# Kernel tuning notes

Measured on AMD Instinct MI355X. Metric: run time of the kernel, lower is better.

Reference implementation:

```python
import jax, jax.numpy as jnp
import numpy as np

BN_EPS = 1e-5
NN_EPS = 1e-8
K = 3


def conv_bn_relu(x, W, b, gamma, beta, mean, var):
    # x: [B, Cin, N]; W: [Cout, Cin] (1x1 conv); BN in inference mode w/ running stats
    y = jnp.einsum('bcn,oc->bon', x, W) + b[None, :, None]
    y = (y - mean[None, :, None]) * (gamma / jnp.sqrt(var + BN_EPS))[None, :, None] + beta[None, :, None]
    return jax.nn.relu(y)


def three_interpolation(p1, p2, f2):
    # p1: [B, N1, 3] unknown xyz; p2: [B, N2, 3] known xyz; f2: [B, C, N2]
    # squared pairwise distances via the expansion trick (avoids [B,N1,N2,3])
    d2 = (jnp.sum(p1 * p1, -1)[:, :, None]
          + jnp.sum(p2 * p2, -1)[:, None, :]
          - 2.0 * jnp.einsum('bnd,bmd->bnm', p1, p2))  # [B, N1, N2]
    neg_d2, idx = jax.lax.top_k(-d2, K)                 # 3 nearest
    dist = -neg_d2                                      # squared dists, [B, N1, 3]
    recip = 1.0 / (dist + NN_EPS)
    weight = recip / jnp.sum(recip, axis=-1, keepdims=True)  # [B, N1, 3]
    f2t = jnp.transpose(f2, (0, 2, 1))                  # [B, N2, C]
    gathered = jax.vmap(lambda f, i: f[i])(f2t, idx)    # [B, N1, 3, C]
    return jnp.einsum('bnkc,bnk->bcn', gathered, weight)  # [B, C, N1]


def setup_inputs() -> dict:
    key = jax.random.key(0)
    ks = jax.random.split(key, 16)
    B, N1, N2 = 8, 16384, 4096
    mlp = [256, 128, 128]
    inp = {
        'p1': jax.random.normal(ks[0], (B, N1, 3), jnp.float32),
        'p2': jax.random.normal(ks[1], (B, N2, 3), jnp.float32),
        'f2': jax.random.normal(ks[2], (B, mlp[0], N2), jnp.float32),
    }
    kidx = 3
    for li in range(len(mlp) - 1):
        cin, cout = mlp[li], mlp[li + 1]
        inp[f'W{li}'] = jax.random.normal(ks[kidx], (cout, cin), jnp.float32) * (1.0 / np.sqrt(cin)); kidx += 1
        inp[f'b{li}'] = jnp.zeros((cout,), jnp.float32)
        inp[f'gamma{li}'] = jnp.ones((cout,), jnp.float32)
        inp[f'beta{li}'] = jnp.zeros((cout,), jnp.float32)
        inp[f'mean{li}'] = jax.random.normal(ks[kidx], (cout,), jnp.float32) * 0.1; kidx += 1
        inp[f'var{li}'] = jax.random.uniform(ks[kidx], (cout,), jnp.float32, 0.5, 1.5); kidx += 1
    return inp


def reference(p1, p2, f2,
              W0, b0, gamma0, beta0, mean0, var0,
              W1, b1, gamma1, beta1, mean1, var1):
    f = conv_bn_relu(f2, W0, b0, gamma0, beta0, mean0, var0)
    f = conv_bn_relu(f, W1, b1, gamma1, beta1, mean1, var1)
    return three_interpolation(p1, p2, f)
```

## Files before the change

### kernel.cpp

```cpp
#include <hip/hip_runtime.h>

#define B_    8
#define N1_   16384
#define N2_   4096
#define NTOT_ (B_ * N1_)

__device__ __forceinline__ float np_sumsq(float x, float y, float z)
{
#pragma clang fp contract(off)
    return ((x * x + y * y) + z * z);
}

__global__ __launch_bounds__(256) void fold_kernel(
    const float* __restrict__ W, const float* __restrict__ bias,
    const float* __restrict__ gamma, const float* __restrict__ beta,
    const float* __restrict__ mean, const float* __restrict__ var,
    float* __restrict__ Wp, float* __restrict__ bp, int Cout, int Cin)
{
    int t = blockIdx.x * 256 + threadIdx.x;
    if (t < Cout * Cin) {
        int o = t / Cin;
        float s = gamma[o] / sqrtf(var[o] + 1e-5f);
        Wp[t] = W[t] * s;
    }
    if (t < Cout) {
        float s = gamma[t] / sqrtf(var[t] + 1e-5f);
        bp[t] = beta[t] + (bias[t] - mean[t]) * s;
    }
}

__global__ __launch_bounds__(256) void q4_kernel(
    const float* __restrict__ p2, float4* __restrict__ q4)
{
    int t = blockIdx.x * 256 + threadIdx.x;
    float x = p2[3 * (size_t)t + 0];
    float y = p2[3 * (size_t)t + 1];
    float z = p2[3 * (size_t)t + 2];
    q4[t] = make_float4(x, y, z, np_sumsq(x, y, z));
}

template <int CIN, bool TRANS>
__global__ __launch_bounds__(256) void gemm_relu_kernel(
    const float* __restrict__ X, const float* __restrict__ Wp,
    const float* __restrict__ bp, float* __restrict__ Y)
{
    __shared__ float A_lds[32][136];
    __shared__ float B_lds[32][128];

    const int b  = blockIdx.y;
    const int n0 = blockIdx.x * 128;
    const int tid = threadIdx.x;
    const int ty = tid >> 4;
    const int tx = tid & 15;
    const float* Xb = X + (size_t)b * CIN * N2_;

    float acc[8][8];
#pragma unroll
    for (int i = 0; i < 8; ++i)
#pragma unroll
        for (int j = 0; j < 8; ++j) acc[i][j] = 0.f;

    const int a_kq = (tid & 7) * 4;
    const int a_r0 = tid >> 3;
    const int b_n4 = (tid & 31) * 4;
    const int b_k0 = tid >> 5;

    for (int k0 = 0; k0 < CIN; k0 += 32) {
#pragma unroll
        for (int i = 0; i < 4; ++i) {
            const int row = a_r0 + 32 * i;
            const float4 v = *(const float4*)&Wp[(size_t)row * CIN + k0 + a_kq];
            A_lds[a_kq + 0][row] = v.x;
            A_lds[a_kq + 1][row] = v.y;
            A_lds[a_kq + 2][row] = v.z;
            A_lds[a_kq + 3][row] = v.w;
        }
#pragma unroll
        for (int i = 0; i < 4; ++i) {
            const int krow = b_k0 + 8 * i;
            *(float4*)&B_lds[krow][b_n4] =
                *(const float4*)&Xb[(size_t)(k0 + krow) * N2_ + n0 + b_n4];
        }
        __syncthreads();

#pragma unroll
        for (int kk = 0; kk < 32; ++kk) {
            const float4 a0 = *(const float4*)&A_lds[kk][ty * 4];
            const float4 a1 = *(const float4*)&A_lds[kk][64 + ty * 4];
            const float4 bq0 = *(const float4*)&B_lds[kk][tx * 4];
            const float4 bq1 = *(const float4*)&B_lds[kk][64 + tx * 4];
            const float av[8] = {a0.x, a0.y, a0.z, a0.w, a1.x, a1.y, a1.z, a1.w};
            const float bv[8] = {bq0.x, bq0.y, bq0.z, bq0.w, bq1.x, bq1.y, bq1.z, bq1.w};
#pragma unroll
            for (int i = 0; i < 8; ++i)
#pragma unroll
                for (int j = 0; j < 8; ++j)
                    acc[i][j] = fmaf(av[i], bv[j], acc[i][j]);
        }
        __syncthreads();
    }

    float bias_v[8];
#pragma unroll
    for (int i = 0; i < 8; ++i) {
        const int r = (i < 4) ? (ty * 4 + i) : (64 + ty * 4 + (i - 4));
        bias_v[i] = bp[r];
    }

    if (!TRANS) {
#pragma unroll
        for (int i = 0; i < 8; ++i) {
            const int r = (i < 4) ? (ty * 4 + i) : (64 + ty * 4 + (i - 4));
            float* yrow = Y + ((size_t)b * 128 + r) * N2_ + n0;
            float4 v0, v1;
            v0.x = fmaxf(acc[i][0] + bias_v[i], 0.f);
            v0.y = fmaxf(acc[i][1] + bias_v[i], 0.f);
            v0.z = fmaxf(acc[i][2] + bias_v[i], 0.f);
            v0.w = fmaxf(acc[i][3] + bias_v[i], 0.f);
            v1.x = fmaxf(acc[i][4] + bias_v[i], 0.f);
            v1.y = fmaxf(acc[i][5] + bias_v[i], 0.f);
            v1.z = fmaxf(acc[i][6] + bias_v[i], 0.f);
            v1.w = fmaxf(acc[i][7] + bias_v[i], 0.f);
            *(float4*)(yrow + tx * 4) = v0;
            *(float4*)(yrow + 64 + tx * 4) = v1;
        }
    } else {
        float (*T)[132] = (float(*)[132])&A_lds[0][0];
#pragma unroll
        for (int s = 0; s < 4; ++s) {
            if ((tx >> 3) == (s & 1)) {
                const int joff = (s >> 1) * 4;
                const int cl0 = (tx & 7) * 4;
#pragma unroll
                for (int i = 0; i < 8; ++i) {
                    const int r = (i < 4) ? (ty * 4 + i) : (64 + ty * 4 + (i - 4));
#pragma unroll
                    for (int j = 0; j < 4; ++j)
                        T[cl0 + j][r] = fmaxf(acc[i][j + joff] + bias_v[i], 0.f);
                }
            }
            __syncthreads();
#pragma unroll
            for (int p = 0; p < 4; ++p) {
                const int row = (tid >> 5) + 8 * p;
                const float4 v = *(const float4*)&T[row][(tid & 31) * 4];
                float* orow = Y + ((size_t)b * N2_ + n0 + 32 * s + row) * 128;
                *(float4*)&orow[(tid & 31) * 4] = v;
            }
            __syncthreads();
        }
    }
}

__global__ __launch_bounds__(256, 8) void knn_phase1(
    const float* __restrict__ p1, const float4* __restrict__ q4,
    float* __restrict__ part_d, int* __restrict__ part_i)
{
    __shared__ float4 qs[1024];
    const int tid = threadIdx.x;
    const int chunk = blockIdx.x & 3;
    const int g = (blockIdx.x >> 2) * 256 + tid;
    const int b = g >> 14;

    const float px = p1[3 * (size_t)g + 0];
    const float py = p1[3 * (size_t)g + 1];
    const float pz = p1[3 * (size_t)g + 2];
    const float s1 = np_sumsq(px, py, pz);

    const float4* qb = q4 + (size_t)b * N2_ + chunk * 1024;
#pragma unroll
    for (int i = 0; i < 4; ++i) qs[tid + i * 256] = qb[tid + i * 256];
    __syncthreads();

    float d0 = 1e30f, d1 = 1e30f, d2v = 1e30f;
    int i0 = 0, i1 = 0, i2 = 0;
    const int jbase = chunk * 1024;

    for (int j = 0; j < 1024; j += 4) {
#pragma unroll
        for (int u = 0; u < 4; ++u) {
            const float4 q = qs[j + u];
            const float dot = __fmaf_rn(px, q.x, __fmaf_rn(py, q.y, __fmul_rn(pz, q.z)));
            const float ss  = s1 + q.w;
            const float t   = __fmaf_rn(-2.0f, dot, ss);
            if (t < d2v) {
                const int jj = jbase + j + u;
                const bool c1 = t < d1, c0 = t < d0;
                d2v = c1 ? d1 : t;                 i2 = c1 ? i1 : jj;
                const float nd1 = c1 ? (c0 ? d0 : t) : d1;
                const int   ni1 = c1 ? (c0 ? i0 : jj) : i1;
                d1 = nd1;                          i1 = ni1;
                d0 = c0 ? t : d0;                  i0 = c0 ? jj : i0;
            }
        }
    }

    part_d[(0 * 4 + chunk) * NTOT_ + g] = d0;
    part_d[(1 * 4 + chunk) * NTOT_ + g] = d1;
    part_d[(2 * 4 + chunk) * NTOT_ + g] = d2v;
    part_i[(0 * 4 + chunk) * NTOT_ + g] = i0;
    part_i[(1 * 4 + chunk) * NTOT_ + g] = i1;
    part_i[(2 * 4 + chunk) * NTOT_ + g] = i2;
}

__global__ __launch_bounds__(256) void knn_merge(
    const float* __restrict__ part_d, const int* __restrict__ part_i,
    int* __restrict__ idx_ws, float* __restrict__ w_ws)
{
    const int g = blockIdx.x * 256 + threadIdx.x;

    float d0 = 1e30f, d1 = 1e30f, d2v = 1e30f;
    int i0 = 0, i1 = 0, i2 = 0;

#pragma unroll
    for (int c = 0; c < 4; ++c) {
#pragma unroll
        for (int k = 0; k < 3; ++k) {
            const float t = part_d[(k * 4 + c) * NTOT_ + g];
            const int  jj = part_i[(k * 4 + c) * NTOT_ + g];
            if (t < d2v) {
                const bool c1 = t < d1, c0 = t < d0;
                d2v = c1 ? d1 : t;                 i2 = c1 ? i1 : jj;
                const float nd1 = c1 ? (c0 ? d0 : t) : d1;
                const int   ni1 = c1 ? (c0 ? i0 : jj) : i1;
                d1 = nd1;                          i1 = ni1;
                d0 = c0 ? t : d0;                  i0 = c0 ? jj : i0;
            }
        }
    }

    float w0, w1, w2;
    {
#pragma clang fp contract(off)
        const float r0 = 1.0f / (d0 + 1e-8f);
        const float r1 = 1.0f / (d1 + 1e-8f);
        const float r2 = 1.0f / (d2v + 1e-8f);
        const float rs = (r0 + r1) + r2;
        w0 = r0 / rs;
        w1 = r1 / rs;
        w2 = r2 / rs;
    }

    idx_ws[g]             = i0;
    idx_ws[NTOT_ + g]     = i1;
    idx_ws[2 * NTOT_ + g] = i2;
    w_ws[g]               = w0;
    w_ws[NTOT_ + g]       = w1;
    w_ws[2 * NTOT_ + g]   = w2;
}

__global__ __launch_bounds__(256) void gather_kernel(
    const float* __restrict__ f_t, const int* __restrict__ idx_ws,
    const float* __restrict__ w_ws, float* __restrict__ out)
{
    const int tid = threadIdx.x;
    const int lane = tid & 63, cg = tid >> 6;
    const int g = blockIdx.x * 64 + lane;
    const int b = g >> 14, n = g & 16383;

    const int i0 = idx_ws[g];
    const int i1 = idx_ws[NTOT_ + g];
    const int i2 = idx_ws[2 * NTOT_ + g];
    const float w0 = w_ws[g];
    const float w1 = w_ws[NTOT_ + g];
    const float w2 = w_ws[2 * NTOT_ + g];

    const float* base = f_t + (size_t)b * N2_ * 128 + cg * 32;
    const float4* r0 = (const float4*)(base + (size_t)i0 * 128);
    const float4* r1 = (const float4*)(base + (size_t)i1 * 128);
    const float4* r2 = (const float4*)(base + (size_t)i2 * 128);

    float acc[32];
#pragma unroll
    for (int q = 0; q < 8; ++q) {
        const float4 a = r0[q], bb = r1[q], c = r2[q];
        acc[4 * q + 0] = fmaf(w0, a.x, fmaf(w1, bb.x, w2 * c.x));
        acc[4 * q + 1] = fmaf(w0, a.y, fmaf(w1, bb.y, w2 * c.y));
        acc[4 * q + 2] = fmaf(w0, a.z, fmaf(w1, bb.z, w2 * c.z));
        acc[4 * q + 3] = fmaf(w0, a.w, fmaf(w1, bb.w, w2 * c.w));
    }

    float* ob = out + ((size_t)b * 128 + cg * 32) * N1_ + n;
#pragma unroll
    for (int c = 0; c < 32; ++c)
        __builtin_nontemporal_store(acc[c], ob + (size_t)c * N1_);
}

extern "C" void kernel_launch(void* const* d_in, const int* in_sizes, int n_in,
                              void* d_out, int out_size, void* d_ws, size_t ws_size,
                              hipStream_t stream)
{
    const float* p1  = (const float*)d_in[0];
    const float* p2  = (const float*)d_in[1];
    const float* f2  = (const float*)d_in[2];
    const float* W0  = (const float*)d_in[3];
    const float* b0  = (const float*)d_in[4];
    const float* g0  = (const float*)d_in[5];
    const float* be0 = (const float*)d_in[6];
    const float* m0  = (const float*)d_in[7];
    const float* v0  = (const float*)d_in[8];
    const float* W1  = (const float*)d_in[9];
    const float* b1  = (const float*)d_in[10];
    const float* g1  = (const float*)d_in[11];
    const float* be1 = (const float*)d_in[12];
    const float* m1  = (const float*)d_in[13];
    const float* v1  = (const float*)d_in[14];

    char* ws = (char*)d_ws;
    float4* q4  = (float4*)(ws);
    float*  W0p = (float*)(ws + (512 << 10));
    float*  b0p = (float*)(ws + (640 << 10));
    float*  W1p = (float*)(ws + (644 << 10));
    float*  b1p = (float*)(ws + (708 << 10));
    float*  h   = (float*)(ws + ((size_t)1 << 20));
    float*  f_t = (float*)(ws + ((size_t)17 << 20));
    int*    idxw= (int*)  (ws + ((size_t)33 << 20));
    float*  wgt = (float*)(ws + ((size_t)35 << 20));
    float*  pd  = (float*)(ws + ((size_t)1 << 20));
    int*    pi  = (int*)  (ws + ((size_t)9 << 20));

    fold_kernel<<<128, 256, 0, stream>>>(W0, b0, g0, be0, m0, v0, W0p, b0p, 128, 256);
    fold_kernel<<<64, 256, 0, stream>>>(W1, b1, g1, be1, m1, v1, W1p, b1p, 128, 128);
    q4_kernel<<<(B_ * N2_) / 256, 256, 0, stream>>>(p2, q4);

    gemm_relu_kernel<256, false><<<dim3(32, 8), 256, 0, stream>>>(f2, W0p, b0p, h);
    gemm_relu_kernel<128, true ><<<dim3(32, 8), 256, 0, stream>>>(h, W1p, b1p, f_t);

    knn_phase1<<<(NTOT_ / 256) * 4, 256, 0, stream>>>(p1, q4, pd, pi);
    knn_merge<<<NTOT_ / 256, 256, 0, stream>>>(pd, pi, idxw, wgt);
    gather_kernel<<<NTOT_ / 64, 256, 0, stream>>>(f_t, idxw, wgt, (float*)d_out);
}
```

Baseline: 352.6 us.

## Fuse prep kernels, make top-3 insert branchless, merge kNN merge into gather

Combines the two BN-fold kernels and the q4 packing kernel into one prep launch. The kNN inner loop's top-3 insertion becomes a fully branchless select chain instead of a guarded branch. The merge step is folded into the gather kernel: one wavefront per block merges the partial candidates into LDS, and a remapped block order spreads work across batches. This drops launches and the idx/weight round trip through global memory, at the cost of 3/4 of each block idling during the merge and extra selects on every candidate in the hot loop.

```diff
diff --git a/kernel.cpp b/kernel.cpp
--- a/kernel.cpp
+++ b/kernel.cpp
@@ -11,32 +11,44 @@
     return ((x * x + y * y) + z * z);
 }
 
-__global__ __launch_bounds__(256) void fold_kernel(
-    const float* __restrict__ W, const float* __restrict__ bias,
-    const float* __restrict__ gamma, const float* __restrict__ beta,
-    const float* __restrict__ mean, const float* __restrict__ var,
-    float* __restrict__ Wp, float* __restrict__ bp, int Cout, int Cin)
-{
-    int t = blockIdx.x * 256 + threadIdx.x;
-    if (t < Cout * Cin) {
-        int o = t / Cin;
-        float s = gamma[o] / sqrtf(var[o] + 1e-5f);
-        Wp[t] = W[t] * s;
-    }
-    if (t < Cout) {
-        float s = gamma[t] / sqrtf(var[t] + 1e-5f);
-        bp[t] = beta[t] + (bias[t] - mean[t]) * s;
-    }
-}
-
-__global__ __launch_bounds__(256) void q4_kernel(
-    const float* __restrict__ p2, float4* __restrict__ q4)
-{
-    int t = blockIdx.x * 256 + threadIdx.x;
-    float x = p2[3 * (size_t)t + 0];
-    float y = p2[3 * (size_t)t + 1];
-    float z = p2[3 * (size_t)t + 2];
-    q4[t] = make_float4(x, y, z, np_sumsq(x, y, z));
+__global__ __launch_bounds__(256) void prep_kernel(
+    const float* __restrict__ p2,
+    const float* __restrict__ W0, const float* __restrict__ b0,
+    const float* __restrict__ g0, const float* __restrict__ be0,
+    const float* __restrict__ m0, const float* __restrict__ v0,
+    const float* __restrict__ W1, const float* __restrict__ b1,
+    const float* __restrict__ g1, const float* __restrict__ be1,
+    const float* __restrict__ m1, const float* __restrict__ v1,
+    float* __restrict__ W0p, float* __restrict__ b0p,
+    float* __restrict__ W1p, float* __restrict__ b1p,
+    float4* __restrict__ q4)
+{
+    const int blk = blockIdx.x, tid = threadIdx.x;
+    if (blk < 128) {
+        const int t = blk * 256 + tid;
+        const int o = t >> 8;
+        const float s = g0[o] / sqrtf(v0[o] + 1e-5f);
+        W0p[t] = W0[t] * s;
+        if (t < 128) {
+            const float sb = g0[t] / sqrtf(v0[t] + 1e-5f);
+            b0p[t] = be0[t] + (b0[t] - m0[t]) * sb;
+        }
+    } else if (blk < 192) {
+        const int t = (blk - 128) * 256 + tid;
+        const int o = t >> 7;
+        const float s = g1[o] / sqrtf(v1[o] + 1e-5f);
+        W1p[t] = W1[t] * s;
+        if (t < 128) {
+            const float sb = g1[t] / sqrtf(v1[t] + 1e-5f);
+            b1p[t] = be1[t] + (b1[t] - m1[t]) * sb;
+        }
+    } else {
+        const int t = (blk - 192) * 256 + tid;
+        const float x = p2[3 * (size_t)t + 0];
+        const float y = p2[3 * (size_t)t + 1];
+        const float z = p2[3 * (size_t)t + 2];
+        q4[t] = make_float4(x, y, z, np_sumsq(x, y, z));
+    }
 }
 
 template <int CIN, bool TRANS>
@@ -183,15 +195,15 @@
             const float dot = __fmaf_rn(px, q.x, __fmaf_rn(py, q.y, __fmul_rn(pz, q.z)));
             const float ss  = s1 + q.w;
             const float t   = __fmaf_rn(-2.0f, dot, ss);
-            if (t < d2v) {
-                const int jj = jbase + j + u;
-                const bool c1 = t < d1, c0 = t < d0;
-                d2v = c1 ? d1 : t;                 i2 = c1 ? i1 : jj;
-                const float nd1 = c1 ? (c0 ? d0 : t) : d1;
-                const int   ni1 = c1 ? (c0 ? i0 : jj) : i1;
-                d1 = nd1;                          i1 = ni1;
-                d0 = c0 ? t : d0;                  i0 = c0 ? jj : i0;
-            }
+            const int jj = jbase + j + u;
+            const bool c0 = t < d0, c1 = t < d1, c2 = t < d2v;
+            const float nd2 = c1 ? d1 : (c2 ? t : d2v);
+            const int   ni2 = c1 ? i1 : (c2 ? jj : i2);
+            const float nd1 = c0 ? d0 : (c1 ? t : d1);
+            const int   ni1 = c0 ? i0 : (c1 ? jj : i1);
+            d0 = c0 ? t : d0;  i0 = c0 ? jj : i0;
+            d1 = nd1;          i1 = ni1;
+            d2v = nd2;         i2 = ni2;
         }
     }
 
@@ -203,67 +215,58 @@
     part_i[(2 * 4 + chunk) * NTOT_ + g] = i2;
 }
 
-__global__ __launch_bounds__(256) void knn_merge(
-    const float* __restrict__ part_d, const int* __restrict__ part_i,
-    int* __restrict__ idx_ws, float* __restrict__ w_ws)
-{
-    const int g = blockIdx.x * 256 + threadIdx.x;
-
-    float d0 = 1e30f, d1 = 1e30f, d2v = 1e30f;
-    int i0 = 0, i1 = 0, i2 = 0;
-
-#pragma unroll
-    for (int c = 0; c < 4; ++c) {
-#pragma unroll
-        for (int k = 0; k < 3; ++k) {
-            const float t = part_d[(k * 4 + c) * NTOT_ + g];
-            const int  jj = part_i[(k * 4 + c) * NTOT_ + g];
-            if (t < d2v) {
-                const bool c1 = t < d1, c0 = t < d0;
-                d2v = c1 ? d1 : t;                 i2 = c1 ? i1 : jj;
-                const float nd1 = c1 ? (c0 ? d0 : t) : d1;
-                const int   ni1 = c1 ? (c0 ? i0 : jj) : i1;
-                d1 = nd1;                          i1 = ni1;
-                d0 = c0 ? t : d0;                  i0 = c0 ? jj : i0;
+__global__ __launch_bounds__(256) void gather_merge_kernel(
+    const float* __restrict__ f_t, const float* __restrict__ part_d,
+    const int* __restrict__ part_i, float* __restrict__ out)
+{
+    __shared__ float wL[3][64];
+    __shared__ int   iL[3][64];
+
+    const int tid = threadIdx.x;
+    const int oldb = (blockIdx.x >> 3) + (blockIdx.x & 7) * 256;
+
+    if (tid < 64) {
+        const int g = oldb * 64 + tid;
+        float d0 = 1e30f, d1 = 1e30f, d2v = 1e30f;
+        int i0 = 0, i1 = 0, i2 = 0;
+#pragma unroll
+        for (int c = 0; c < 4; ++c) {
+#pragma unroll
+            for (int k = 0; k < 3; ++k) {
+                const float t = part_d[(k * 4 + c) * NTOT_ + g];
+                const int  jj = part_i[(k * 4 + c) * NTOT_ + g];
+                if (t < d2v) {
+                    const bool c1 = t < d1, c0 = t < d0;
+                    d2v = c1 ? d1 : t;                 i2 = c1 ? i1 : jj;
+                    const float nd1 = c1 ? (c0 ? d0 : t) : d1;
+                    const int   ni1 = c1 ? (c0 ? i0 : jj) : i1;
+                    d1 = nd1;                          i1 = ni1;
+                    d0 = c0 ? t : d0;                  i0 = c0 ? jj : i0;
+                }
             }
         }
-    }
-
-    float w0, w1, w2;
-    {
+        float w0, w1, w2;
+        {
 #pragma clang fp contract(off)
-        const float r0 = 1.0f / (d0 + 1e-8f);
-        const float r1 = 1.0f / (d1 + 1e-8f);
-        const float r2 = 1.0f / (d2v + 1e-8f);
-        const float rs = (r0 + r1) + r2;
-        w0 = r0 / rs;
-        w1 = r1 / rs;
-        w2 = r2 / rs;
-    }
-
-    idx_ws[g]             = i0;
-    idx_ws[NTOT_ + g]     = i1;
-    idx_ws[2 * NTOT_ + g] = i2;
-    w_ws[g]               = w0;
-    w_ws[NTOT_ + g]       = w1;
-    w_ws[2 * NTOT_ + g]   = w2;
-}
-
-__global__ __launch_bounds__(256) void gather_kernel(
-    const float* __restrict__ f_t, const int* __restrict__ idx_ws,
-    const float* __restrict__ w_ws, float* __restrict__ out)
-{
-    const int tid = threadIdx.x;
+            const float r0 = 1.0f / (d0 + 1e-8f);
+            const float r1 = 1.0f / (d1 + 1e-8f);
+            const float r2 = 1.0f / (d2v + 1e-8f);
+            const float rs = (r0 + r1) + r2;
+            w0 = r0 / rs;
+            w1 = r1 / rs;
+            w2 = r2 / rs;
+        }
+        wL[0][tid] = w0; wL[1][tid] = w1; wL[2][tid] = w2;
+        iL[0][tid] = i0; iL[1][tid] = i1; iL[2][tid] = i2;
+    }
+    __syncthreads();
+
     const int lane = tid & 63, cg = tid >> 6;
-    const int g = blockIdx.x * 64 + lane;
+    const int g = oldb * 64 + lane;
     const int b = g >> 14, n = g & 16383;
 
-    const int i0 = idx_ws[g];
-    const int i1 = idx_ws[NTOT_ + g];
-    const int i2 = idx_ws[2 * NTOT_ + g];
-    const float w0 = w_ws[g];
-    const float w1 = w_ws[NTOT_ + g];
-    const float w2 = w_ws[2 * NTOT_ + g];
+    const int i0 = iL[0][lane], i1 = iL[1][lane], i2 = iL[2][lane];
+    const float w0 = wL[0][lane], w1 = wL[1][lane], w2 = wL[2][lane];
 
     const float* base = f_t + (size_t)b * N2_ * 128 + cg * 32;
     const float4* r0 = (const float4*)(base + (size_t)i0 * 128);
@@ -314,19 +317,16 @@
     float*  b1p = (float*)(ws + (708 << 10));
     float*  h   = (float*)(ws + ((size_t)1 << 20));
     float*  f_t = (float*)(ws + ((size_t)17 << 20));
-    int*    idxw= (int*)  (ws + ((size_t)33 << 20));
-    float*  wgt = (float*)(ws + ((size_t)35 << 20));
     float*  pd  = (float*)(ws + ((size_t)1 << 20));
     int*    pi  = (int*)  (ws + ((size_t)9 << 20));
 
-    fold_kernel<<<128, 256, 0, stream>>>(W0, b0, g0, be0, m0, v0, W0p, b0p, 128, 256);
-    fold_kernel<<<64, 256, 0, stream>>>(W1, b1, g1, be1, m1, v1, W1p, b1p, 128, 128);
-    q4_kernel<<<(B_ * N2_) / 256, 256, 0, stream>>>(p2, q4);
+    prep_kernel<<<320, 256, 0, stream>>>(p2,
+        W0, b0, g0, be0, m0, v0, W1, b1, g1, be1, m1, v1,
+        W0p, b0p, W1p, b1p, q4);
 
     gemm_relu_kernel<256, false><<<dim3(32, 8), 256, 0, stream>>>(f2, W0p, b0p, h);
     gemm_relu_kernel<128, true ><<<dim3(32, 8), 256, 0, stream>>>(h, W1p, b1p, f_t);
 
     knn_phase1<<<(NTOT_ / 256) * 4, 256, 0, stream>>>(p1, q4, pd, pi);
-    knn_merge<<<NTOT_ / 256, 256, 0, stream>>>(pd, pi, idxw, wgt);
-    gather_kernel<<<NTOT_ / 64, 256, 0, stream>>>(f_t, idxw, wgt, (float*)d_out);
-}
+    gather_merge_kernel<<<NTOT_ / 64, 256, 0, stream>>>(f_t, pd, pi, (float*)d_out);
+}
```

New measurement: 440.5 us. 1.25x slower.
